# Optimization experiments

Hardware: AMD Instinct MI355X
Metric: run time of the kernel (lower is better)

## Reference

```python
import jax, jax.numpy as jnp
import numpy as np

def _round_ste(x):
    # StraightThrough: forward = round, backward = identity
    return x + jax.lax.stop_gradient(jnp.round(x) - x)

def setup_inputs() -> dict:
    key = jax.random.key(0)
    k1, k2, k3, k4, k5 = jax.random.split(key, 5)
    in_f, out_f, n_tok = 4096, 4096, 8192
    return {
        "input": jax.random.normal(k1, (n_tok, in_f), dtype=jnp.float32),
        "weight": jax.random.normal(k2, (out_f, in_f), dtype=jnp.float32),
        "bias": jax.random.normal(k3, (out_f,), dtype=jnp.float32),
        "w_scale": jax.random.uniform(k4, (1,), dtype=jnp.float32),
        "b_scale": jax.random.uniform(k5, (1,), dtype=jnp.float32),
    }

def reference(input, weight, bias, w_scale, b_scale):
    # straight-through rounding of quantized latents (use_straight_through=True, compress_bias=True)
    w_q = _round_ste(weight)
    b_q = _round_ste(bias)
    # decoder: per-tensor affine dequantization
    w_dec = w_scale * w_q          # [out, in]
    b_dec = b_scale * b_q          # [out]
    # F.linear: input @ weight.T + bias
    return jnp.einsum('ni,oi->no', input, w_dec) + b_dec
```

## Files before the change

### kernel.cpp

```cpp
#include <hip/hip_runtime.h>
#include <stdint.h>


using bf16x8  = __attribute__((ext_vector_type(8))) __bf16;
using floatx4 = __attribute__((ext_vector_type(4))) float;
using us8     = __attribute__((ext_vector_type(8))) unsigned short;
using us4     = __attribute__((ext_vector_type(4))) unsigned short;

__device__ __forceinline__ unsigned short f2bf_rne(float x) {
    unsigned int u = __float_as_uint(x);
    return (unsigned short)((u + 0x7fffu + ((u >> 16) & 1u)) >> 16);
}

__device__ __forceinline__ void load_lds16(const unsigned short* g, unsigned short* l) {
    __builtin_amdgcn_global_load_lds(
        (__attribute__((address_space(1))) void*)g,
        (__attribute__((address_space(3))) void*)l,
        16, 0, 0);
}

__global__ __launch_bounds__(256) void cvt_both(
    const float* __restrict__ inA, unsigned short* __restrict__ outA, long long nA4,
    const float* __restrict__ inB, unsigned short* __restrict__ outB, long long nB4) {
    const long long i = (long long)blockIdx.x * 256 + threadIdx.x;
    if (i < nA4) {
        float4 v = ((const float4*)inA)[i];
        us4 o = { f2bf_rne(v.x), f2bf_rne(v.y), f2bf_rne(v.z), f2bf_rne(v.w) };
        ((us4*)outA)[i] = o;
    } else {
        const long long j = i - nA4;
        if (j < nB4) {
            float4 v = ((const float4*)inB)[j];
            us4 o = { f2bf_rne(rintf(v.x)), f2bf_rne(rintf(v.y)),
                      f2bf_rne(rintf(v.z)), f2bf_rne(rintf(v.w)) };
            ((us4*)outB)[j] = o;
        }
    }
}

__global__ __launch_bounds__(256) void gemm_bf16_bt(
    const unsigned short* __restrict__ A,
    const unsigned short* __restrict__ B,
    const float* __restrict__ bias,
    const float* __restrict__ wscale_p,
    const float* __restrict__ bscale_p,
    float* __restrict__ C,
    int M, int N, int K) {
    constexpr int BM = 128, BK = 32;
    __shared__ unsigned short ldsA[BM * BK];
    __shared__ unsigned short ldsB[BM * BK];

    const int tid  = threadIdx.x;
    const int wave = tid >> 6;
    const int lane = tid & 63;
    const int quad = lane >> 4;
    const int l16  = lane & 15;

    const int bm = blockIdx.y * BM;
    const int bn = blockIdx.x * BM;
    const int wm = (wave >> 1) * 64;
    const int wn = (wave & 1) * 64;

    const float wsc = wscale_p[0];
    const float bsc = bscale_p[0];

    float badd[4];
#pragma unroll
    for (int ni = 0; ni < 4; ++ni)
        badd[ni] = bsc * rintf(bias[bn + wn + ni * 16 + l16]);

    const int r0 = wave * 32 + (lane >> 2);
    const int kc = ((lane & 3) ^ ((lane >> 3) & 3)) * 8;
    const unsigned short* gA0 = A + (size_t)(bm + r0) * K + kc;
    const unsigned short* gA1 = A + (size_t)(bm + r0 + 16) * K + kc;
    const unsigned short* gB0 = B + (size_t)(bn + r0) * K + kc;
    const unsigned short* gB1 = B + (size_t)(bn + r0 + 16) * K + kc;
    unsigned short* lA0 = &ldsA[(wave * 128 + 0) * 8];
    unsigned short* lA1 = &ldsA[(wave * 128 + 64) * 8];
    unsigned short* lB0 = &ldsB[(wave * 128 + 0) * 8];
    unsigned short* lB1 = &ldsB[(wave * 128 + 64) * 8];

    const int xr = (l16 >> 1) & 3;
    const int sa = (quad ^ xr) * 8;

    floatx4 acc[4][4] = {};

    for (int kt = 0; kt < K; kt += BK) {
        load_lds16(gA0 + kt, lA0);
        load_lds16(gA1 + kt, lA1);
        load_lds16(gB0 + kt, lB0);
        load_lds16(gB1 + kt, lB1);
        __syncthreads();

        bf16x8 af[4], bfr[4];
#pragma unroll
        for (int mi = 0; mi < 4; ++mi) {
            const int off = (wm + mi * 16 + l16) * BK + sa;
            af[mi] = __builtin_bit_cast(bf16x8, *(const us8*)&ldsA[off]);
        }
#pragma unroll
        for (int ni = 0; ni < 4; ++ni) {
            const int off = (wn + ni * 16 + l16) * BK + sa;
            bfr[ni] = __builtin_bit_cast(bf16x8, *(const us8*)&ldsB[off]);
        }
#pragma unroll
        for (int mi = 0; mi < 4; ++mi)
#pragma unroll
            for (int ni = 0; ni < 4; ++ni)
                acc[mi][ni] = __builtin_amdgcn_mfma_f32_16x16x32_bf16(
                    af[mi], bfr[ni], acc[mi][ni], 0, 0, 0);
        __syncthreads();
    }

#pragma unroll
    for (int mi = 0; mi < 4; ++mi) {
        const int m0 = bm + wm + mi * 16 + quad * 4;
#pragma unroll
        for (int ni = 0; ni < 4; ++ni) {
            const int n = bn + wn + ni * 16 + l16;
#pragma unroll
            for (int r = 0; r < 4; ++r)
                C[(size_t)(m0 + r) * N + n] = acc[mi][ni][r] * wsc + badd[ni];
        }
    }
}

__global__ __launch_bounds__(256) void fallback_gemm(
    const float* __restrict__ A, const float* __restrict__ W,
    const float* __restrict__ bias, const float* __restrict__ wsp,
    const float* __restrict__ bsp, float* __restrict__ C, int M, int N, int K) {
    const int n = blockIdx.x * 256 + threadIdx.x;
    const int m = blockIdx.y;
    if (n >= N || m >= M) return;
    float s = 0.f;
    for (int k = 0; k < K; ++k)
        s += A[(size_t)m * K + k] * rintf(W[(size_t)n * K + k]);
    C[(size_t)m * N + n] = s * wsp[0] + bsp[0] * rintf(bias[n]);
}

extern "C" void kernel_launch(void* const* d_in, const int* in_sizes, int n_in,
                              void* d_out, int out_size, void* d_ws, size_t ws_size,
                              hipStream_t stream) {
    const float* input  = (const float*)d_in[0];
    const float* weight = (const float*)d_in[1];
    const float* bias   = (const float*)d_in[2];
    const float* wscale = (const float*)d_in[3];
    const float* bscale = (const float*)d_in[4];
    float* out = (float*)d_out;

    const int N = in_sizes[2];
    const int K = in_sizes[1] / N;
    const int M = in_sizes[0] / K;

    const size_t needA = (size_t)M * K * sizeof(unsigned short);
    const size_t needB = (size_t)N * K * sizeof(unsigned short);

    if (ws_size >= needA + needB && (M % 128) == 0 && (N % 128) == 0 &&
        (K % 32) == 0) {
        unsigned short* Abf = (unsigned short*)d_ws;
        unsigned short* Bbf = (unsigned short*)((char*)d_ws + needA);
        const long long nA4 = (long long)M * K / 4;
        const long long nB4 = (long long)N * K / 4;
        const long long nthr = nA4 + nB4;
        cvt_both<<<(unsigned)((nthr + 255) / 256), 256, 0, stream>>>(
            input, Abf, nA4, weight, Bbf, nB4);
        dim3 grid(N / 128, M / 128);
        gemm_bf16_bt<<<grid, 256, 0, stream>>>(Abf, Bbf, bias, wscale, bscale, out, M, N, K);
    } else {
        dim3 grid((N + 255) / 256, M);
        fallback_gemm<<<grid, 256, 0, stream>>>(input, weight, bias, wscale, bscale, out, M, N, K);
    }
}
```

Measured before the change: 594.6 us.

## Switch GEMM to 32x32x16 MFMA with BK=64 and 8-way XOR swizzle

Replaces the 16x16x32 bf16 MFMA tiling with 32x32x16 MFMA instructions, so each wave computes its 64x64 tile as 2x2 larger fragments. It also doubles the K tile to 64, which halves the number of barrier pairs per K sweep, and uses an 8-way XOR swizzle for the LDS layout. The aim is fewer LDS fragment reads and fewer barriers per MFMA. In exchange, LDS use doubles, the epilogue store pattern changes, and the fast path now requires K to be a multiple of 64.

```diff
diff --git a/kernel.cpp b/kernel.cpp
--- a/kernel.cpp
+++ b/kernel.cpp
@@ -2,10 +2,10 @@
 #include <stdint.h>
 
 
-using bf16x8  = __attribute__((ext_vector_type(8))) __bf16;
-using floatx4 = __attribute__((ext_vector_type(4))) float;
-using us8     = __attribute__((ext_vector_type(8))) unsigned short;
-using us4     = __attribute__((ext_vector_type(4))) unsigned short;
+using bf16x8   = __attribute__((ext_vector_type(8))) __bf16;
+using floatx16 = __attribute__((ext_vector_type(16))) float;
+using us8      = __attribute__((ext_vector_type(8))) unsigned short;
+using us4      = __attribute__((ext_vector_type(4))) unsigned short;
 
 __device__ __forceinline__ unsigned short f2bf_rne(float x) {
     unsigned int u = __float_as_uint(x);
@@ -46,15 +46,13 @@
     const float* __restrict__ bscale_p,
     float* __restrict__ C,
     int M, int N, int K) {
-    constexpr int BM = 128, BK = 32;
+    constexpr int BM = 128, BK = 64;
     __shared__ unsigned short ldsA[BM * BK];
     __shared__ unsigned short ldsB[BM * BK];
 
     const int tid  = threadIdx.x;
     const int wave = tid >> 6;
     const int lane = tid & 63;
-    const int quad = lane >> 4;
-    const int l16  = lane & 15;
 
     const int bm = blockIdx.y * BM;
     const int bn = blockIdx.x * BM;
@@ -64,63 +62,74 @@
     const float wsc = wscale_p[0];
     const float bsc = bscale_p[0];
 
-    float badd[4];
+    const int col = lane & 31;
+    const int khalf = lane >> 5;
+
+    float badd[2];
 #pragma unroll
-    for (int ni = 0; ni < 4; ++ni)
-        badd[ni] = bsc * rintf(bias[bn + wn + ni * 16 + l16]);
+    for (int ni = 0; ni < 2; ++ni)
+        badd[ni] = bsc * rintf(bias[bn + wn + ni * 32 + col]);
 
-    const int r0 = wave * 32 + (lane >> 2);
-    const int kc = ((lane & 3) ^ ((lane >> 3) & 3)) * 8;
-    const unsigned short* gA0 = A + (size_t)(bm + r0) * K + kc;
-    const unsigned short* gA1 = A + (size_t)(bm + r0 + 16) * K + kc;
-    const unsigned short* gB0 = B + (size_t)(bn + r0) * K + kc;
-    const unsigned short* gB1 = B + (size_t)(bn + r0 + 16) * K + kc;
-    unsigned short* lA0 = &ldsA[(wave * 128 + 0) * 8];
-    unsigned short* lA1 = &ldsA[(wave * 128 + 64) * 8];
-    unsigned short* lB0 = &ldsB[(wave * 128 + 0) * 8];
-    unsigned short* lB1 = &ldsB[(wave * 128 + 64) * 8];
+    const int g_st = ((lane & 7) ^ (lane >> 3)) * 8;
+    const unsigned short* gAp[4];
+    const unsigned short* gBp[4];
+    unsigned short* lA[4];
+    unsigned short* lB[4];
+#pragma unroll
+    for (int i = 0; i < 4; ++i) {
+        const int r = wave * 32 + i * 8 + (lane >> 3);
+        gAp[i] = A + (size_t)(bm + r) * K + g_st;
+        gBp[i] = B + (size_t)(bn + r) * K + g_st;
+        lA[i] = &ldsA[(wave * 256 + i * 64) * 8];
+        lB[i] = &ldsB[(wave * 256 + i * 64) * 8];
+    }
 
-    const int xr = (l16 >> 1) & 3;
-    const int sa = (quad ^ xr) * 8;
-
-    floatx4 acc[4][4] = {};
+    floatx16 acc[2][2] = {};
 
     for (int kt = 0; kt < K; kt += BK) {
-        load_lds16(gA0 + kt, lA0);
-        load_lds16(gA1 + kt, lA1);
-        load_lds16(gB0 + kt, lB0);
-        load_lds16(gB1 + kt, lB1);
+#pragma unroll
+        for (int i = 0; i < 4; ++i) {
+            load_lds16(gAp[i] + kt, lA[i]);
+            load_lds16(gBp[i] + kt, lB[i]);
+        }
         __syncthreads();
 
-        bf16x8 af[4], bfr[4];
 #pragma unroll
-        for (int mi = 0; mi < 4; ++mi) {
-            const int off = (wm + mi * 16 + l16) * BK + sa;
-            af[mi] = __builtin_bit_cast(bf16x8, *(const us8*)&ldsA[off]);
+        for (int ks = 0; ks < 4; ++ks) {
+            const int gc = ks * 2 + khalf;
+            const int slot = (gc ^ (lane & 7)) * 8;
+            bf16x8 af[2], bfr[2];
+#pragma unroll
+            for (int mi = 0; mi < 2; ++mi) {
+                const int off = (wm + mi * 32 + col) * BK + slot;
+                af[mi] = __builtin_bit_cast(bf16x8, *(const us8*)&ldsA[off]);
+            }
+#pragma unroll
+            for (int ni = 0; ni < 2; ++ni) {
+                const int off = (wn + ni * 32 + col) * BK + slot;
+                bfr[ni] = __builtin_bit_cast(bf16x8, *(const us8*)&ldsB[off]);
+            }
+#pragma unroll
+            for (int mi = 0; mi < 2; ++mi)
+#pragma unroll
+                for (int ni = 0; ni < 2; ++ni)
+                    acc[mi][ni] = __builtin_amdgcn_mfma_f32_32x32x16_bf16(
+                        af[mi], bfr[ni], acc[mi][ni], 0, 0, 0);
         }
-#pragma unroll
-        for (int ni = 0; ni < 4; ++ni) {
-            const int off = (wn + ni * 16 + l16) * BK + sa;
-            bfr[ni] = __builtin_bit_cast(bf16x8, *(const us8*)&ldsB[off]);
-        }
-#pragma unroll
-        for (int mi = 0; mi < 4; ++mi)
-#pragma unroll
-            for (int ni = 0; ni < 4; ++ni)
-                acc[mi][ni] = __builtin_amdgcn_mfma_f32_16x16x32_bf16(
-                    af[mi], bfr[ni], acc[mi][ni], 0, 0, 0);
         __syncthreads();
     }
 
+    const int rbase = 4 * khalf;
 #pragma unroll
-    for (int mi = 0; mi < 4; ++mi) {
-        const int m0 = bm + wm + mi * 16 + quad * 4;
+    for (int mi = 0; mi < 2; ++mi) {
 #pragma unroll
-        for (int ni = 0; ni < 4; ++ni) {
-            const int n = bn + wn + ni * 16 + l16;
+        for (int ni = 0; ni < 2; ++ni) {
+            const int n = bn + wn + ni * 32 + col;
 #pragma unroll
-            for (int r = 0; r < 4; ++r)
-                C[(size_t)(m0 + r) * N + n] = acc[mi][ni][r] * wsc + badd[ni];
+            for (int reg = 0; reg < 16; ++reg) {
+                const int m = bm + wm + mi * 32 + (reg & 3) + 8 * (reg >> 2) + rbase;
+                C[(size_t)m * N + n] = acc[mi][ni][reg] * wsc + badd[ni];
+            }
         }
     }
 }
@@ -156,7 +165,7 @@
     const size_t needB = (size_t)N * K * sizeof(unsigned short);
 
     if (ws_size >= needA + needB && (M % 128) == 0 && (N % 128) == 0 &&
-        (K % 32) == 0) {
+        (K % 64) == 0) {
         unsigned short* Abf = (unsigned short*)d_ws;
         unsigned short* Bbf = (unsigned short*)((char*)d_ws + needA);
         const long long nA4 = (long long)M * K / 4;
```

New measurement: 533.5 us. -10.3%, faster.
